# Kernel tuning notes

Measured on AMD Instinct MI355X. Metric: run time of the kernel, lower is better.

## Reference

```python
import jax, jax.numpy as jnp
import numpy as np
from jax import lax

V, E, H1, H2, D = 10000, 128, 128, 64, 64
T, B, MAXLEN = 512, 256, 30
SOS, EOS = 1, 2


def setup_inputs() -> dict:
    key = jax.random.key(0)
    ks = jax.random.split(key, 16)
    s = 0.05
    return {
        "enc_key": jax.random.normal(ks[0], (T, B, D), jnp.float32),
        "enc_values": jax.random.normal(ks[1], (T, B, D), jnp.float32),
        "mask": jax.random.randint(ks[2], (B, 1, T), 0, 2, jnp.int32),
        "emb": jax.random.normal(ks[3], (V, E), jnp.float32) * s,
        "w_ih1": jax.random.normal(ks[4], (4 * H1, E + D), jnp.float32) * s,
        "w_hh1": jax.random.normal(ks[5], (4 * H1, H1), jnp.float32) * s,
        "b_ih1": jax.random.normal(ks[6], (4 * H1,), jnp.float32) * s,
        "b_hh1": jax.random.normal(ks[7], (4 * H1,), jnp.float32) * s,
        "w_ih2": jax.random.normal(ks[8], (4 * H2, H1), jnp.float32) * s,
        "w_hh2": jax.random.normal(ks[9], (4 * H2, H2), jnp.float32) * s,
        "b_ih2": jax.random.normal(ks[10], (4 * H2,), jnp.float32) * s,
        "b_hh2": jax.random.normal(ks[11], (4 * H2,), jnp.float32) * s,
        "wq": jax.random.normal(ks[12], (D, H2), jnp.float32) * s,
        "bq": jax.random.normal(ks[13], (D,), jnp.float32) * s,
        "wp": jax.random.normal(ks[14], (V, H2 + D), jnp.float32) * s,
        "bp": jax.random.normal(ks[15], (V,), jnp.float32) * s,
    }


def _lstm_cell(x, h, c, w_ih, w_hh, b_ih, b_hh):
    # torch LSTMCell: gates ordered (i, f, g, o)
    gates = x @ w_ih.T + h @ w_hh.T + b_ih + b_hh
    i, f, g, o = jnp.split(gates, 4, axis=-1)
    c_new = jax.nn.sigmoid(f) * c + jax.nn.sigmoid(i) * jnp.tanh(g)
    h_new = jax.nn.sigmoid(o) * jnp.tanh(c_new)
    return h_new, c_new


def reference(enc_key, enc_values, mask, emb, w_ih1, w_hh1, b_ih1, b_hh1,
              w_ih2, w_hh2, b_ih2, b_hh2, wq, bq, wp, bp):
    maskf = mask.astype(enc_key.dtype)[:, 0, :]          # (B, T)
    emb_p = emb.at[EOS].set(0.0)                          # padding_idx row zeroed

    pred0 = jnp.zeros((B, V), enc_key.dtype).at[:, SOS].set(1.0)
    init = (jnp.zeros((B, H1), enc_key.dtype), jnp.zeros((B, H1), enc_key.dtype),
            jnp.zeros((B, H2), enc_key.dtype), jnp.zeros((B, H2), enc_key.dtype),
            jnp.zeros((B, D), enc_key.dtype), pred0)

    def step(carry, _):
        h1, c1, h2, c2, context, pred = carry
        tok = jnp.argmax(pred, axis=-1)                   # greedy feedback
        char_embed = emb_p[tok]                           # (B, E)
        inp = jnp.concatenate([char_embed, context], axis=1)
        h1, c1 = _lstm_cell(inp, h1, c1, w_ih1, w_hh1, b_ih1, b_hh1)
        h2, c2 = _lstm_cell(h1, h2, c2, w_ih2, w_hh2, b_ih2, b_hh2)
        query = h2 @ wq.T + bq                            # (B, D)
        energy = jnp.einsum('bd,tbd->bt', query, enc_key)
        att = jax.nn.softmax(energy, axis=-1)
        m_att = maskf * att
        m_att = m_att / jnp.clip(jnp.sum(m_att, axis=-1, keepdims=True), 2e-30, None)
        context = jnp.einsum('bt,tbd->bd', m_att, enc_values)
        pred = jnp.concatenate([h2, context], axis=1) @ wp.T + bp
        return (h1, c1, h2, c2, context, pred), pred

    _, preds = lax.scan(step, init, None, length=MAXLEN)  # (MAXLEN, B, V)
    return jnp.transpose(preds, (1, 0, 2))                # (B, MAXLEN, V)
```

## Files before the change

### kernel.cpp

```cpp
#include <hip/hip_runtime.h>
#include <hip/hip_bf16.h>

#define V 10000
#define E 128
#define H1 128
#define H2 64
#define D 64
#define T 512
#define B 256
#define MAXLEN 30
#define SOS 1
#define EOS 2
#define BGS 8
#define NVB 40

#define O_EMB   0
#define O_WIH1  1280000
#define O_WHH1  1378304
#define O_BIH1  1443840
#define O_BHH1  1444352
#define O_WIH2  1444864
#define O_WHH2  1477632
#define O_BIH2  1494016
#define O_BHH2  1494272
#define O_WQ    1494528
#define O_BQ    1498624
#define O_WP    1498688
#define O_BP    2778688
#define TOTALW  2788688

typedef unsigned long long u64;

__device__ __forceinline__ float bl(unsigned u){ return __uint_as_float(u << 16); }
__device__ __forceinline__ float bh(unsigned u){ return __uint_as_float(u & 0xFFFF0000u); }
__device__ __forceinline__ float b2f(__hip_bfloat16 x){ return __bfloat162float(x); }
__device__ __forceinline__ float sigf(float x){ return 1.f/(1.f + expf(-x)); }

__device__ __forceinline__ uint4 ldu4(const void* p){
  uint4 r; __builtin_memcpy(&r, p, 16); return r;
}
__device__ __forceinline__ float4 ldf4(const float* p){
  float4 r; __builtin_memcpy(&r, (const void*)p, 16); return r;
}
__device__ __forceinline__ float dot8b(const float* x, uint4 w){
  return x[0]*bl(w.x) + x[1]*bh(w.x) + x[2]*bl(w.y) + x[3]*bh(w.y)
       + x[4]*bl(w.z) + x[5]*bh(w.z) + x[6]*bl(w.w) + x[7]*bh(w.w);
}
__device__ __forceinline__ float dot4f(const float* x, float4 w){
  return x[0]*w.x + x[1]*w.y + x[2]*w.z + x[3]*w.w;
}

__global__ void kdtype(const void* __restrict__ probe, int* __restrict__ flagp){
  const int tid = threadIdx.x;
  const unsigned w = ((const unsigned*)probe)[tid];
  const unsigned e = (w >> 7) & 0xFFu;
  const bool inband = (e >= 0x60u) && (e <= 0x7Eu);
  const u64 m = __ballot(inband);
  if (tid == 0) flagp[0] = (m == 0xFFFFFFFFFFFFFFFFull) ? 1 : 0;
}

__global__ __launch_bounds__(256) void kcvt(
    const void* s_emb, const void* s_wih1, const void* s_whh1,
    const void* s_bih1, const void* s_bhh1, const void* s_wih2,
    const void* s_whh2, const void* s_bih2, const void* s_bhh2,
    const void* s_wq, const void* s_bq, const void* s_wp, const void* s_bp,
    float* __restrict__ dst, const int* __restrict__ flagp)
{
  const int idx = blockIdx.x * 256 + threadIdx.x;
  if (idx >= TOTALW) return;
  const int flag = flagp[0];
  const void* src; int off;
  if      (idx < O_WIH1){ src = s_emb;  off = idx - O_EMB;  }
  else if (idx < O_WHH1){ src = s_wih1; off = idx - O_WIH1; }
  else if (idx < O_BIH1){ src = s_whh1; off = idx - O_WHH1; }
  else if (idx < O_BHH1){ src = s_bih1; off = idx - O_BIH1; }
  else if (idx < O_WIH2){ src = s_bhh1; off = idx - O_BHH1; }
  else if (idx < O_WHH2){ src = s_wih2; off = idx - O_WIH2; }
  else if (idx < O_BIH2){ src = s_whh2; off = idx - O_WHH2; }
  else if (idx < O_BHH2){ src = s_bih2; off = idx - O_BIH2; }
  else if (idx < O_WQ)  { src = s_bhh2; off = idx - O_BHH2; }
  else if (idx < O_BQ)  { src = s_wq;   off = idx - O_WQ;   }
  else if (idx < O_WP)  { src = s_bq;   off = idx - O_BQ;   }
  else if (idx < O_BP)  { src = s_wp;   off = idx - O_WP;   }
  else                  { src = s_bp;   off = idx - O_BP;   }
  dst[idx] = flag ? b2f(((const __hip_bfloat16*)src)[off])
                  : ((const float*)src)[off];
}

__global__ __launch_bounds__(256) void kdec(
    int t,
    const void* __restrict__ enc_key,
    const void* __restrict__ enc_val,
    const int* __restrict__ mask,
    const float* __restrict__ emb_f,
    const float* __restrict__ wih1_f, const float* __restrict__ whh1_f,
    const float* __restrict__ bih1_f, const float* __restrict__ bhh1_f,
    const float* __restrict__ wih2_f, const float* __restrict__ whh2_f,
    const float* __restrict__ bih2_f, const float* __restrict__ bhh2_f,
    const float* __restrict__ wq_f,   const float* __restrict__ bq_f,
    float* __restrict__ h1, float* __restrict__ c1,
    float* __restrict__ h2, float* __restrict__ c2,
    float* __restrict__ ctx, float* __restrict__ xvec,
    const float* __restrict__ candv, const int* __restrict__ candi,
    const int* __restrict__ flagp)
{
  const int b = blockIdx.x;
  const int tid = threadIdx.x;
  const int flagb = flagp[0];

  __shared__ float inp_s[E + D];
  __shared__ float h1_s[H1];
  __shared__ float h2_s[H2];
  __shared__ float g_s[4*H1];
  __shared__ float q_s[D];
  __shared__ float wv_s[T];
  __shared__ float red_s[256];
  __shared__ float cv_s[NVB];
  __shared__ int   ci_s[NVB];
  __shared__ int   tok_s;

  if (t > 0 && tid < NVB){
    cv_s[tid] = candv[b*NVB + tid];
    ci_s[tid] = candi[b*NVB + tid];
  }
  __syncthreads();
  if (tid == 0){
    int tok = SOS;
    if (t > 0){
      float bv = cv_s[0]; int bi = ci_s[0];
      for (int j = 1; j < NVB; ++j)
        if (cv_s[j] > bv){ bv = cv_s[j]; bi = ci_s[j]; }
      tok = bi;
    }
    tok_s = tok;
  }
  __syncthreads();
  const int tok = tok_s;

  if (tid < E){
    inp_s[tid] = (tok == EOS) ? 0.f : emb_f[(size_t)tok*E + tid];
  } else if (tid < E + D){
    inp_s[tid] = (t == 0) ? 0.f : ctx[b*D + (tid - E)];
  }
  if (tid < H1)                h1_s[tid]       = (t == 0) ? 0.f : h1[b*H1 + tid];
  if (tid >= 128 && tid < 192) h2_s[tid - 128] = (t == 0) ? 0.f : h2[b*H2 + (tid - 128)];
  __syncthreads();

  for (int j = tid; j < 4*H1; j += 256){
    const float* wr = wih1_f + (size_t)j*(E + D);
    float acc = bih1_f[j] + bhh1_f[j];
    #pragma unroll
    for (int kk = 0; kk < (E + D)/4; ++kk) acc += dot4f(inp_s + kk*4, ldf4(wr + kk*4));
    const float* wr2 = whh1_f + (size_t)j*H1;
    #pragma unroll
    for (int kk = 0; kk < H1/4; ++kk) acc += dot4f(h1_s + kk*4, ldf4(wr2 + kk*4));
    g_s[j] = acc;
  }
  __syncthreads();

  if (tid < H1){
    float gi = sigf(g_s[tid]);
    float gf = sigf(g_s[H1 + tid]);
    float gg = tanhf(g_s[2*H1 + tid]);
    float go = sigf(g_s[3*H1 + tid]);
    float cold = (t == 0) ? 0.f : c1[b*H1 + tid];
    float cn = gf*cold + gi*gg;
    float hn = go*tanhf(cn);
    c1[b*H1 + tid] = cn;
    h1[b*H1 + tid] = hn;
    h1_s[tid] = hn;
  }
  __syncthreads();

  {
    const int j = tid;
    const float* wr = wih2_f + (size_t)j*H1;
    float acc = bih2_f[j] + bhh2_f[j];
    #pragma unroll
    for (int kk = 0; kk < H1/4; ++kk) acc += dot4f(h1_s + kk*4, ldf4(wr + kk*4));
    const float* wr2 = whh2_f + (size_t)j*H2;
    #pragma unroll
    for (int kk = 0; kk < H2/4; ++kk) acc += dot4f(h2_s + kk*4, ldf4(wr2 + kk*4));
    g_s[j] = acc;
  }
  __syncthreads();

  if (tid < H2){
    float gi = sigf(g_s[tid]);
    float gf = sigf(g_s[H2 + tid]);
    float gg = tanhf(g_s[2*H2 + tid]);
    float go = sigf(g_s[3*H2 + tid]);
    float cold = (t == 0) ? 0.f : c2[b*H2 + tid];
    float cn = gf*cold + gi*gg;
    float hn = go*tanhf(cn);
    c2[b*H2 + tid] = cn;
    h2[b*H2 + tid] = hn;
    h2_s[tid] = hn;
    xvec[b*(H2 + D) + tid] = hn;
  }
  __syncthreads();

  if (tid < D){
    const float* wr = wq_f + (size_t)tid*H2;
    float acc = bq_f[tid];
    #pragma unroll
    for (int kk = 0; kk < H2/4; ++kk) acc += dot4f(h2_s + kk*4, ldf4(wr + kk*4));
    q_s[tid] = acc;
  }
  __syncthreads();

  float e0 = 0.f, e1 = 0.f;
  if (flagb){
    const __hip_bfloat16* base = (const __hip_bfloat16*)enc_key;
    const __hip_bfloat16* kr0 = base + ((size_t)tid*B + b)*D;
    const __hip_bfloat16* kr1 = base + ((size_t)(tid + 256)*B + b)*D;
    #pragma unroll
    for (int kk = 0; kk < D/8; ++kk){
      e0 += dot8b(q_s + kk*8, ldu4(kr0 + kk*8));
      e1 += dot8b(q_s + kk*8, ldu4(kr1 + kk*8));
    }
  } else {
    const float* base = (const float*)enc_key;
    const float* kr0 = base + ((size_t)tid*B + b)*D;
    const float* kr1 = base + ((size_t)(tid + 256)*B + b)*D;
    #pragma unroll
    for (int kk = 0; kk < D/4; ++kk){
      e0 += dot4f(q_s + kk*4, ldf4(kr0 + kk*4));
      e1 += dot4f(q_s + kk*4, ldf4(kr1 + kk*4));
    }
  }
  red_s[tid] = fmaxf(e0, e1);
  __syncthreads();
  for (int s = 128; s > 0; s >>= 1){
    if (tid < s) red_s[tid] = fmaxf(red_s[tid], red_s[tid + s]);
    __syncthreads();
  }
  const float emax = red_s[0];
  __syncthreads();

  const int m0 = mask[b*T + tid], m1 = mask[b*T + tid + 256];
  const float w0 = m0 ? expf(e0 - emax) : 0.f;
  const float w1 = m1 ? expf(e1 - emax) : 0.f;
  wv_s[tid] = w0;
  wv_s[tid + 256] = w1;
  red_s[tid] = w0 + w1;
  __syncthreads();
  for (int s = 128; s > 0; s >>= 1){
    if (tid < s) red_s[tid] += red_s[tid + s];
    __syncthreads();
  }
  const float inv = 1.f / fmaxf(red_s[0], 2e-30f);
  __syncthreads();

  {
    const int d = tid & 63, ch = tid >> 6;
    float acc = 0.f;
    if (flagb){
      const __hip_bfloat16* base = (const __hip_bfloat16*)enc_val;
      for (int tt = ch*128; tt < ch*128 + 128; ++tt)
        acc += wv_s[tt] * b2f(base[((size_t)tt*B + b)*D + d]);
    } else {
      const float* base = (const float*)enc_val;
      for (int tt = ch*128; tt < ch*128 + 128; ++tt)
        acc += wv_s[tt] * base[((size_t)tt*B + b)*D + d];
    }
    red_s[tid] = acc;
  }
  __syncthreads();
  if (tid < D){
    float cv = (red_s[tid] + red_s[tid + 64] + red_s[tid + 128] + red_s[tid + 192]) * inv;
    ctx[b*D + tid] = cv;
    xvec[b*(H2 + D) + H2 + tid] = cv;
  }
}

__global__ __launch_bounds__(256) void kpred(
    int t,
    const float* __restrict__ wp_f,
    const float* __restrict__ bp_f,
    const float* __restrict__ xvec,
    void* __restrict__ outv,
    float* __restrict__ candv, int* __restrict__ candi,
    const int* __restrict__ flagp)
{
  const int tid = threadIdx.x;
  const int vb = blockIdx.x;
  const int v = vb * 256 + tid;
  const int bg = blockIdx.y;
  const int flagb = flagp[0];
  const bool valid = v < V;
  const int vc = valid ? v : 0;
  const float* wrow = wp_f + (size_t)vc*(H2 + D);
  const float* xp = xvec + (size_t)bg*BGS*(H2 + D);

  float acc[BGS];
  #pragma unroll
  for (int i = 0; i < BGS; ++i) acc[i] = 0.f;

  #pragma unroll
  for (int kk = 0; kk < (H2 + D)/4; ++kk){
    const float4 w = ldf4(wrow + kk*4);
    #pragma unroll
    for (int i = 0; i < BGS; ++i){
      const float* x = xp + i*(H2 + D) + kk*4;
      acc[i] += x[0]*w.x + x[1]*w.y + x[2]*w.z + x[3]*w.w;
    }
  }

  const float bias = valid ? bp_f[vc] : 0.f;
  #pragma unroll
  for (int i = 0; i < BGS; ++i){
    acc[i] += bias;
    if (valid){
      const size_t oi = ((size_t)(bg*BGS + i)*MAXLEN + t)*V + v;
      if (flagb) ((__hip_bfloat16*)outv)[oi] = __float2bfloat16(acc[i]);
      else       ((float*)outv)[oi] = acc[i];
    }
  }

  __shared__ float lv[4][BGS];
  __shared__ int   li[4][BGS];
  const int lane = tid & 63, wid = tid >> 6;
  #pragma unroll
  for (int i = 0; i < BGS; ++i){
    float mv = valid ? acc[i] : -__builtin_inff();
    int   mi = valid ? v : 0x7FFFFFFF;
    for (int off = 32; off > 0; off >>= 1){
      float ov = __shfl_down(mv, off);
      int   oi = __shfl_down(mi, off);
      if (ov > mv || (ov == mv && oi < mi)){ mv = ov; mi = oi; }
    }
    if (lane == 0){ lv[wid][i] = mv; li[wid][i] = mi; }
  }
  __syncthreads();
  if (tid < BGS){
    float mv = lv[0][tid]; int mi = li[0][tid];
    #pragma unroll
    for (int w2 = 1; w2 < 4; ++w2){
      float ov = lv[w2][tid]; int oi = li[w2][tid];
      if (ov > mv || (ov == mv && oi < mi)){ mv = ov; mi = oi; }
    }
    const int b = bg*BGS + tid;
    candv[b*NVB + vb] = mv;
    candi[b*NVB + vb] = mi;
  }
}

extern "C" void kernel_launch(void* const* d_in, const int* in_sizes, int n_in,
                              void* d_out, int out_size, void* d_ws, size_t ws_size,
                              hipStream_t stream)
{
  const void* enc_key = d_in[0];
  const void* enc_val = d_in[1];
  const int*  mask    = (const int*)d_in[2];
  const void* emb     = d_in[3];
  const void* w_ih1   = d_in[4];
  const void* w_hh1   = d_in[5];
  const void* b_ih1   = d_in[6];
  const void* b_hh1   = d_in[7];
  const void* w_ih2   = d_in[8];
  const void* w_hh2   = d_in[9];
  const void* b_ih2   = d_in[10];
  const void* b_hh2   = d_in[11];
  const void* wq      = d_in[12];
  const void* bq      = d_in[13];
  const void* wp      = d_in[14];
  const void* bp      = d_in[15];

  float* wsf  = (float*)d_ws;
  int*  flagp = (int*)wsf;
  float* wts  = wsf + 16;
  float* h1    = wts + TOTALW;
  float* c1    = h1   + B*H1;
  float* h2    = c1   + B*H1;
  float* c2    = h2   + B*H2;
  float* ctx   = c2   + B*H2;
  float* xvec  = ctx  + B*D;
  float* candv = xvec + B*(H2 + D);
  int*   candi = (int*)(candv + B*NVB);

  kdtype<<<dim3(1), dim3(64), 0, stream>>>(b_ih1, flagp);
  kcvt<<<dim3((TOTALW + 255)/256), dim3(256), 0, stream>>>(
      emb, w_ih1, w_hh1, b_ih1, b_hh1, w_ih2, w_hh2, b_ih2, b_hh2,
      wq, bq, wp, bp, wts, flagp);

  for (int t = 0; t < MAXLEN; ++t){
    kdec<<<dim3(B), dim3(256), 0, stream>>>(
        t, enc_key, enc_val, mask,
        wts + O_EMB,
        wts + O_WIH1, wts + O_WHH1, wts + O_BIH1, wts + O_BHH1,
        wts + O_WIH2, wts + O_WHH2, wts + O_BIH2, wts + O_BHH2,
        wts + O_WQ, wts + O_BQ,
        h1, c1, h2, c2, ctx, xvec, candv, candi, flagp);
    kpred<<<dim3(NVB, B/BGS), dim3(256), 0, stream>>>(
        t, wts + O_WP, wts + O_BP, xvec, d_out, candv, candi, flagp);
  }
}
```

Measured before the change: 3.816 ms.

## Fuse decoder steps into one persistent kernel with grid barriers

Replaces the 60 per-step launches with a single persistent kernel of 256 blocks that loops over all 30 timesteps and uses a software grid barrier between phases. The LSTM weights are partitioned across blocks and held in shared memory, so each block computes a slice of gates for a group of batch rows instead of rereading every weight row per batch. A separate pre-pass transposes the encoder keys and values to a batch-major fp32 layout for contiguous attention reads, and logits are written with nontemporal stores. The persistent design assumes all 256 blocks are co-resident and relies on a spin-wait barrier with a timeout fallback, which adds a deadlock and correctness risk.

Result: slower. 8.181 ms (+114.4%).

```diff
diff --git a/kernel.cpp b/kernel.cpp
--- a/kernel.cpp
+++ b/kernel.cpp
@@ -13,6 +13,7 @@
 #define EOS 2
 #define BGS 8
 #define NVB 40
+#define NBLK 256
 
 #define O_EMB   0
 #define O_WIH1  1280000
@@ -31,23 +32,33 @@
 
 typedef unsigned long long u64;
 
-__device__ __forceinline__ float bl(unsigned u){ return __uint_as_float(u << 16); }
-__device__ __forceinline__ float bh(unsigned u){ return __uint_as_float(u & 0xFFFF0000u); }
 __device__ __forceinline__ float b2f(__hip_bfloat16 x){ return __bfloat162float(x); }
 __device__ __forceinline__ float sigf(float x){ return 1.f/(1.f + expf(-x)); }
-
-__device__ __forceinline__ uint4 ldu4(const void* p){
-  uint4 r; __builtin_memcpy(&r, p, 16); return r;
-}
 __device__ __forceinline__ float4 ldf4(const float* p){
   float4 r; __builtin_memcpy(&r, (const void*)p, 16); return r;
 }
-__device__ __forceinline__ float dot8b(const float* x, uint4 w){
-  return x[0]*bl(w.x) + x[1]*bh(w.x) + x[2]*bl(w.y) + x[3]*bh(w.y)
-       + x[4]*bl(w.z) + x[5]*bh(w.z) + x[6]*bl(w.w) + x[7]*bh(w.w);
-}
 __device__ __forceinline__ float dot4f(const float* x, float4 w){
   return x[0]*w.x + x[1]*w.y + x[2]*w.z + x[3]*w.w;
+}
+
+__device__ __forceinline__ void gsync(unsigned* bar){
+  __syncthreads();
+  __threadfence();
+  if (threadIdx.x == 0){
+    const unsigned ticket = __hip_atomic_fetch_add(bar, 1u, __ATOMIC_ACQ_REL, __HIP_MEMORY_SCOPE_AGENT);
+    const unsigned target = ticket - (ticket % (unsigned)NBLK) + (unsigned)NBLK;
+    unsigned spins = 0u;
+    while (__hip_atomic_load(bar, __ATOMIC_RELAXED, __HIP_MEMORY_SCOPE_AGENT) < target){
+      if (__hip_atomic_load(bar + 1, __ATOMIC_RELAXED, __HIP_MEMORY_SCOPE_AGENT) != 0u) break;
+      if (++spins > 30000000u){
+        __hip_atomic_store(bar + 1, 1u, __ATOMIC_RELAXED, __HIP_MEMORY_SCOPE_AGENT);
+        break;
+      }
+      __builtin_amdgcn_s_sleep(1);
+    }
+  }
+  __syncthreads();
+  __threadfence();
 }
 
 __global__ void kdtype(const void* __restrict__ probe, int* __restrict__ flagp){
@@ -87,262 +98,333 @@
                   : ((const float*)src)[off];
 }
 
-__global__ __launch_bounds__(256) void kdec(
-    int t,
-    const void* __restrict__ enc_key,
-    const void* __restrict__ enc_val,
-    const int* __restrict__ mask,
-    const float* __restrict__ emb_f,
-    const float* __restrict__ wih1_f, const float* __restrict__ whh1_f,
-    const float* __restrict__ bih1_f, const float* __restrict__ bhh1_f,
-    const float* __restrict__ wih2_f, const float* __restrict__ whh2_f,
-    const float* __restrict__ bih2_f, const float* __restrict__ bhh2_f,
-    const float* __restrict__ wq_f,   const float* __restrict__ bq_f,
-    float* __restrict__ h1, float* __restrict__ c1,
-    float* __restrict__ h2, float* __restrict__ c2,
-    float* __restrict__ ctx, float* __restrict__ xvec,
-    const float* __restrict__ candv, const int* __restrict__ candi,
-    const int* __restrict__ flagp)
+__global__ __launch_bounds__(256) void ktrans(
+    const void* __restrict__ enc_key, const void* __restrict__ enc_val,
+    float* __restrict__ encTk, float* __restrict__ encTv,
+    const int* __restrict__ flagp, unsigned* __restrict__ bar)
 {
   const int b = blockIdx.x;
   const int tid = threadIdx.x;
+  if (b == 0 && tid < 16) bar[tid] = 0u;
+  const int flag = flagp[0];
+  const int d = tid & 63, tq = tid >> 6;
+  if (flag){
+    const __hip_bfloat16* bk = (const __hip_bfloat16*)enc_key;
+    const __hip_bfloat16* bv = (const __hip_bfloat16*)enc_val;
+    for (int tt = tq; tt < T; tt += 4){
+      encTk[((size_t)b*T + tt)*D + d] = b2f(bk[((size_t)tt*B + b)*D + d]);
+      encTv[((size_t)b*T + tt)*D + d] = b2f(bv[((size_t)tt*B + b)*D + d]);
+    }
+  } else {
+    const float* fk = (const float*)enc_key;
+    const float* fv = (const float*)enc_val;
+    for (int tt = tq; tt < T; tt += 4){
+      encTk[((size_t)b*T + tt)*D + d] = fk[((size_t)tt*B + b)*D + d];
+      encTv[((size_t)b*T + tt)*D + d] = fv[((size_t)tt*B + b)*D + d];
+    }
+  }
+}
+
+__global__ __launch_bounds__(256) void kmain(
+    const float* __restrict__ wts,
+    const float* __restrict__ encTk, const float* __restrict__ encTv,
+    const int* __restrict__ mask,
+    void* __restrict__ outv,
+    float* __restrict__ h1g,
+    float* __restrict__ h2g,
+    float* __restrict__ ctxg,
+    float* __restrict__ candv, int* __restrict__ candi,
+    unsigned* __restrict__ bar, const int* __restrict__ flagp)
+{
+  const int bid = blockIdx.x;
+  const int tid = threadIdx.x;
   const int flagb = flagp[0];
 
-  __shared__ float inp_s[E + D];
-  __shared__ float h1_s[H1];
-  __shared__ float h2_s[H2];
-  __shared__ float g_s[4*H1];
+  const int rt  = bid >> 5;
+  const int bA  = (bid & 31) * 8;
+  const int rt2 = bid >> 6;
+  const int bB  = (bid & 63) * 4;
+
+  __shared__ float4 wA4[80*64];
+  __shared__ float4 wB4[48*64];
+  __shared__ __align__(16) float xs[8*324];
+  __shared__ __align__(16) float x2s[4*196];
+  __shared__ float g_s[64*8];
+  __shared__ float c1_s[16*8];
+  __shared__ float c2_s[16*4];
+  __shared__ float bias1_s[64], bias2_s[64];
   __shared__ float q_s[D];
+  __shared__ float h2b_s[H2];
   __shared__ float wv_s[T];
   __shared__ float red_s[256];
-  __shared__ float cv_s[NVB];
-  __shared__ int   ci_s[NVB];
-  __shared__ int   tok_s;
-
-  if (t > 0 && tid < NVB){
-    cv_s[tid] = candv[b*NVB + tid];
-    ci_s[tid] = candi[b*NVB + tid];
-  }
-  __syncthreads();
-  if (tid == 0){
-    int tok = SOS;
+  __shared__ float lv_s[4*8]; __shared__ int li_s[4*8];
+  __shared__ int tok_s[8];
+
+  for (int idx = tid; idx < 80*64; idx += 256){
+    const int k4 = idx >> 6, r = idx & 63;
+    const int row = ((r >> 4) * 128) + (rt * 16) + (r & 15);
+    float4 w;
+    if (k4 < 48) w = ldf4(wts + O_WIH1 + (size_t)row*(E+D) + k4*4);
+    else         w = ldf4(wts + O_WHH1 + (size_t)row*H1 + (k4-48)*4);
+    wA4[idx] = w;
+  }
+  for (int idx = tid; idx < 48*64; idx += 256){
+    const int k4 = idx >> 6, r = idx & 63;
+    const int row = ((r >> 4) * 64) + (rt2 * 16) + (r & 15);
+    float4 w;
+    if (k4 < 32) w = ldf4(wts + O_WIH2 + (size_t)row*H1 + k4*4);
+    else         w = ldf4(wts + O_WHH2 + (size_t)row*H2 + (k4-32)*4);
+    wB4[idx] = w;
+  }
+  if (tid < 64){
+    const int rowA = ((tid >> 4) * 128) + (rt * 16) + (tid & 15);
+    bias1_s[tid] = wts[O_BIH1 + rowA] + wts[O_BHH1 + rowA];
+    const int rowB = ((tid >> 4) * 64) + (rt2 * 16) + (tid & 15);
+    bias2_s[tid] = wts[O_BIH2 + rowB] + wts[O_BHH2 + rowB];
+  }
+  if (tid < 128) c1_s[tid] = 0.f;
+  if (tid < 64)  c2_s[tid] = 0.f;
+  {
+    const int b = bid;
+    if (tid < H1) h1g[(size_t)B*H1 + (size_t)b*H1 + tid] = 0.f;
+    if (tid < H2) h2g[(size_t)B*H2 + (size_t)b*H2 + tid] = 0.f;
+    if (tid < D)  ctxg[(size_t)b*D + tid] = 0.f;
+  }
+  gsync(bar);
+
+  for (int t = 0; t < MAXLEN; ++t){
+    const int par = t & 1;
+    const float* h1prev = h1g + (size_t)(par^1)*B*H1;
+    float*       h1new  = h1g + (size_t)par*B*H1;
+    const float* h2prev = h2g + (size_t)(par^1)*B*H2;
+    float*       h2new  = h2g + (size_t)par*B*H2;
+
     if (t > 0){
-      float bv = cv_s[0]; int bi = ci_s[0];
-      for (int j = 1; j < NVB; ++j)
-        if (cv_s[j] > bv){ bv = cv_s[j]; bi = ci_s[j]; }
-      tok = bi;
-    }
-    tok_s = tok;
-  }
-  __syncthreads();
-  const int tok = tok_s;
-
-  if (tid < E){
-    inp_s[tid] = (tok == EOS) ? 0.f : emb_f[(size_t)tok*E + tid];
-  } else if (tid < E + D){
-    inp_s[tid] = (t == 0) ? 0.f : ctx[b*D + (tid - E)];
-  }
-  if (tid < H1)                h1_s[tid]       = (t == 0) ? 0.f : h1[b*H1 + tid];
-  if (tid >= 128 && tid < 192) h2_s[tid - 128] = (t == 0) ? 0.f : h2[b*H2 + (tid - 128)];
-  __syncthreads();
-
-  for (int j = tid; j < 4*H1; j += 256){
-    const float* wr = wih1_f + (size_t)j*(E + D);
-    float acc = bih1_f[j] + bhh1_f[j];
-    #pragma unroll
-    for (int kk = 0; kk < (E + D)/4; ++kk) acc += dot4f(inp_s + kk*4, ldf4(wr + kk*4));
-    const float* wr2 = whh1_f + (size_t)j*H1;
-    #pragma unroll
-    for (int kk = 0; kk < H1/4; ++kk) acc += dot4f(h1_s + kk*4, ldf4(wr2 + kk*4));
-    g_s[j] = acc;
-  }
-  __syncthreads();
-
-  if (tid < H1){
-    float gi = sigf(g_s[tid]);
-    float gf = sigf(g_s[H1 + tid]);
-    float gg = tanhf(g_s[2*H1 + tid]);
-    float go = sigf(g_s[3*H1 + tid]);
-    float cold = (t == 0) ? 0.f : c1[b*H1 + tid];
-    float cn = gf*cold + gi*gg;
-    float hn = go*tanhf(cn);
-    c1[b*H1 + tid] = cn;
-    h1[b*H1 + tid] = hn;
-    h1_s[tid] = hn;
-  }
-  __syncthreads();
-
-  {
-    const int j = tid;
-    const float* wr = wih2_f + (size_t)j*H1;
-    float acc = bih2_f[j] + bhh2_f[j];
-    #pragma unroll
-    for (int kk = 0; kk < H1/4; ++kk) acc += dot4f(h1_s + kk*4, ldf4(wr + kk*4));
-    const float* wr2 = whh2_f + (size_t)j*H2;
-    #pragma unroll
-    for (int kk = 0; kk < H2/4; ++kk) acc += dot4f(h2_s + kk*4, ldf4(wr2 + kk*4));
-    g_s[j] = acc;
-  }
-  __syncthreads();
-
-  if (tid < H2){
-    float gi = sigf(g_s[tid]);
-    float gf = sigf(g_s[H2 + tid]);
-    float gg = tanhf(g_s[2*H2 + tid]);
-    float go = sigf(g_s[3*H2 + tid]);
-    float cold = (t == 0) ? 0.f : c2[b*H2 + tid];
-    float cn = gf*cold + gi*gg;
-    float hn = go*tanhf(cn);
-    c2[b*H2 + tid] = cn;
-    h2[b*H2 + tid] = hn;
-    h2_s[tid] = hn;
-    xvec[b*(H2 + D) + tid] = hn;
-  }
-  __syncthreads();
-
-  if (tid < D){
-    const float* wr = wq_f + (size_t)tid*H2;
-    float acc = bq_f[tid];
-    #pragma unroll
-    for (int kk = 0; kk < H2/4; ++kk) acc += dot4f(h2_s + kk*4, ldf4(wr + kk*4));
-    q_s[tid] = acc;
-  }
-  __syncthreads();
-
-  float e0 = 0.f, e1 = 0.f;
-  if (flagb){
-    const __hip_bfloat16* base = (const __hip_bfloat16*)enc_key;
-    const __hip_bfloat16* kr0 = base + ((size_t)tid*B + b)*D;
-    const __hip_bfloat16* kr1 = base + ((size_t)(tid + 256)*B + b)*D;
-    #pragma unroll
-    for (int kk = 0; kk < D/8; ++kk){
-      e0 += dot8b(q_s + kk*8, ldu4(kr0 + kk*8));
-      e1 += dot8b(q_s + kk*8, ldu4(kr1 + kk*8));
-    }
-  } else {
-    const float* base = (const float*)enc_key;
-    const float* kr0 = base + ((size_t)tid*B + b)*D;
-    const float* kr1 = base + ((size_t)(tid + 256)*B + b)*D;
-    #pragma unroll
-    for (int kk = 0; kk < D/4; ++kk){
-      e0 += dot4f(q_s + kk*4, ldf4(kr0 + kk*4));
-      e1 += dot4f(q_s + kk*4, ldf4(kr1 + kk*4));
-    }
-  }
-  red_s[tid] = fmaxf(e0, e1);
-  __syncthreads();
-  for (int s = 128; s > 0; s >>= 1){
-    if (tid < s) red_s[tid] = fmaxf(red_s[tid], red_s[tid + s]);
+      const int bi = tid >> 5, j = tid & 31;
+      const int b = bA + bi;
+      float mv = candv[b*NVB + j];
+      int   mi = candi[b*NVB + j];
+      if (j < NVB - 32){
+        float ov = candv[b*NVB + j + 32]; int oi = candi[b*NVB + j + 32];
+        if (ov > mv || (ov == mv && oi < mi)){ mv = ov; mi = oi; }
+      }
+      #pragma unroll
+      for (int off = 16; off > 0; off >>= 1){
+        float ov = __shfl_down(mv, off); int oi = __shfl_down(mi, off);
+        if (ov > mv || (ov == mv && oi < mi)){ mv = ov; mi = oi; }
+      }
+      if (j == 0) tok_s[bi] = mi;
+    } else {
+      if (tid < 8) tok_s[tid] = SOS;
+    }
     __syncthreads();
-  }
-  const float emax = red_s[0];
-  __syncthreads();
-
-  const int m0 = mask[b*T + tid], m1 = mask[b*T + tid + 256];
-  const float w0 = m0 ? expf(e0 - emax) : 0.f;
-  const float w1 = m1 ? expf(e1 - emax) : 0.f;
-  wv_s[tid] = w0;
-  wv_s[tid + 256] = w1;
-  red_s[tid] = w0 + w1;
-  __syncthreads();
-  for (int s = 128; s > 0; s >>= 1){
-    if (tid < s) red_s[tid] += red_s[tid + s];
+
+    for (int bi = 0; bi < 8; ++bi){
+      const int b = bA + bi;
+      const int tok = tok_s[bi];
+      for (int k = tid; k < 320; k += 256){
+        float x;
+        if (k < E)          x = (tok == EOS) ? 0.f : wts[O_EMB + (size_t)tok*E + k];
+        else if (k < E + D) x = ctxg[(size_t)b*D + (k - E)];
+        else                x = h1prev[(size_t)b*H1 + (k - (E + D))];
+        xs[bi*324 + k] = x;
+      }
+    }
     __syncthreads();
-  }
-  const float inv = 1.f / fmaxf(red_s[0], 2e-30f);
-  __syncthreads();
-
-  {
-    const int d = tid & 63, ch = tid >> 6;
-    float acc = 0.f;
-    if (flagb){
-      const __hip_bfloat16* base = (const __hip_bfloat16*)enc_val;
-      for (int tt = ch*128; tt < ch*128 + 128; ++tt)
-        acc += wv_s[tt] * b2f(base[((size_t)tt*B + b)*D + d]);
-    } else {
-      const float* base = (const float*)enc_val;
-      for (int tt = ch*128; tt < ch*128 + 128; ++tt)
-        acc += wv_s[tt] * base[((size_t)tt*B + b)*D + d];
-    }
-    red_s[tid] = acc;
-  }
-  __syncthreads();
-  if (tid < D){
-    float cv = (red_s[tid] + red_s[tid + 64] + red_s[tid + 128] + red_s[tid + 192]) * inv;
-    ctx[b*D + tid] = cv;
-    xvec[b*(H2 + D) + H2 + tid] = cv;
-  }
-}
-
-__global__ __launch_bounds__(256) void kpred(
-    int t,
-    const float* __restrict__ wp_f,
-    const float* __restrict__ bp_f,
-    const float* __restrict__ xvec,
-    void* __restrict__ outv,
-    float* __restrict__ candv, int* __restrict__ candi,
-    const int* __restrict__ flagp)
-{
-  const int tid = threadIdx.x;
-  const int vb = blockIdx.x;
-  const int v = vb * 256 + tid;
-  const int bg = blockIdx.y;
-  const int flagb = flagp[0];
-  const bool valid = v < V;
-  const int vc = valid ? v : 0;
-  const float* wrow = wp_f + (size_t)vc*(H2 + D);
-  const float* xp = xvec + (size_t)bg*BGS*(H2 + D);
-
-  float acc[BGS];
-  #pragma unroll
-  for (int i = 0; i < BGS; ++i) acc[i] = 0.f;
-
-  #pragma unroll
-  for (int kk = 0; kk < (H2 + D)/4; ++kk){
-    const float4 w = ldf4(wrow + kk*4);
-    #pragma unroll
-    for (int i = 0; i < BGS; ++i){
-      const float* x = xp + i*(H2 + D) + kk*4;
-      acc[i] += x[0]*w.x + x[1]*w.y + x[2]*w.z + x[3]*w.w;
-    }
-  }
-
-  const float bias = valid ? bp_f[vc] : 0.f;
-  #pragma unroll
-  for (int i = 0; i < BGS; ++i){
-    acc[i] += bias;
-    if (valid){
-      const size_t oi = ((size_t)(bg*BGS + i)*MAXLEN + t)*V + v;
-      if (flagb) ((__hip_bfloat16*)outv)[oi] = __float2bfloat16(acc[i]);
-      else       ((float*)outv)[oi] = acc[i];
-    }
-  }
-
-  __shared__ float lv[4][BGS];
-  __shared__ int   li[4][BGS];
-  const int lane = tid & 63, wid = tid >> 6;
-  #pragma unroll
-  for (int i = 0; i < BGS; ++i){
-    float mv = valid ? acc[i] : -__builtin_inff();
-    int   mi = valid ? v : 0x7FFFFFFF;
-    for (int off = 32; off > 0; off >>= 1){
-      float ov = __shfl_down(mv, off);
-      int   oi = __shfl_down(mi, off);
-      if (ov > mv || (ov == mv && oi < mi)){ mv = ov; mi = oi; }
-    }
-    if (lane == 0){ lv[wid][i] = mv; li[wid][i] = mi; }
-  }
-  __syncthreads();
-  if (tid < BGS){
-    float mv = lv[0][tid]; int mi = li[0][tid];
-    #pragma unroll
-    for (int w2 = 1; w2 < 4; ++w2){
-      float ov = lv[w2][tid]; int oi = li[w2][tid];
-      if (ov > mv || (ov == mv && oi < mi)){ mv = ov; mi = oi; }
-    }
-    const int b = bg*BGS + tid;
-    candv[b*NVB + vb] = mv;
-    candi[b*NVB + vb] = mi;
+
+    {
+      const int r = tid >> 2, bq = tid & 3;
+      const float4* x0 = (const float4*)(xs + (bq*2    )*324);
+      const float4* x1 = (const float4*)(xs + (bq*2 + 1)*324);
+      float a0 = bias1_s[r], a1 = a0;
+      #pragma unroll 8
+      for (int k4 = 0; k4 < 80; ++k4){
+        const float4 w = wA4[k4*64 + r];
+        const float4 xa = x0[k4], xb = x1[k4];
+        a0 += xa.x*w.x + xa.y*w.y + xa.z*w.z + xa.w*w.w;
+        a1 += xb.x*w.x + xb.y*w.y + xb.z*w.z + xb.w*w.w;
+      }
+      g_s[r*8 + bq*2]     = a0;
+      g_s[r*8 + bq*2 + 1] = a1;
+    }
+    __syncthreads();
+    if (tid < 128){
+      const int ui = tid >> 3, bi = tid & 7;
+      const float gi = sigf (g_s[(ui     )*8 + bi]);
+      const float gf = sigf (g_s[(16 + ui)*8 + bi]);
+      const float gg = tanhf(g_s[(32 + ui)*8 + bi]);
+      const float go = sigf (g_s[(48 + ui)*8 + bi]);
+      const float cn = gf * c1_s[ui*8 + bi] + gi * gg;
+      c1_s[ui*8 + bi] = cn;
+      h1new[(size_t)(bA + bi)*H1 + rt*16 + ui] = go * tanhf(cn);
+    }
+    gsync(bar);
+
+    {
+      const int bi = tid >> 6, k0 = tid & 63;
+      #pragma unroll
+      for (int kk = k0; kk < 192; kk += 64){
+        float x = (kk < H1) ? h1new[(size_t)(bB + bi)*H1 + kk]
+                            : h2prev[(size_t)(bB + bi)*H2 + (kk - H1)];
+        x2s[bi*196 + kk] = x;
+      }
+    }
+    __syncthreads();
+    {
+      const int r = tid >> 2, bq = tid & 3;
+      const float4* xp = (const float4*)(x2s + bq*196);
+      float a = bias2_s[r];
+      #pragma unroll 8
+      for (int k4 = 0; k4 < 48; ++k4){
+        const float4 w = wB4[k4*64 + r];
+        const float4 x = xp[k4];
+        a += x.x*w.x + x.y*w.y + x.z*w.z + x.w*w.w;
+      }
+      g_s[r*8 + bq] = a;
+    }
+    __syncthreads();
+    if (tid < 64){
+      const int ui = tid >> 2, bi = tid & 3;
+      const float gi = sigf (g_s[(ui     )*8 + bi]);
+      const float gf = sigf (g_s[(16 + ui)*8 + bi]);
+      const float gg = tanhf(g_s[(32 + ui)*8 + bi]);
+      const float go = sigf (g_s[(48 + ui)*8 + bi]);
+      const float cn = gf * c2_s[ui*4 + bi] + gi * gg;
+      c2_s[ui*4 + bi] = cn;
+      h2new[(size_t)(bB + bi)*H2 + rt2*16 + ui] = go * tanhf(cn);
+    }
+    gsync(bar);
+
+    {
+      const int b = bid;
+      if (tid < H2) h2b_s[tid] = h2new[(size_t)b*H2 + tid];
+      __syncthreads();
+      if (tid < D){
+        const float* wr = wts + O_WQ + (size_t)tid*H2;
+        float acc = wts[O_BQ + tid];
+        #pragma unroll
+        for (int kk = 0; kk < H2/4; ++kk) acc += dot4f(h2b_s + kk*4, ldf4(wr + kk*4));
+        q_s[tid] = acc;
+      }
+      __syncthreads();
+      float e0 = 0.f, e1 = 0.f;
+      const float* kr0 = encTk + ((size_t)b*T + tid)*D;
+      const float* kr1 = kr0 + (size_t)256*D;
+      #pragma unroll
+      for (int kk = 0; kk < D/4; ++kk){
+        e0 += dot4f(q_s + kk*4, ldf4(kr0 + kk*4));
+        e1 += dot4f(q_s + kk*4, ldf4(kr1 + kk*4));
+      }
+      red_s[tid] = fmaxf(e0, e1);
+      __syncthreads();
+      for (int s = 128; s > 0; s >>= 1){
+        if (tid < s) red_s[tid] = fmaxf(red_s[tid], red_s[tid + s]);
+        __syncthreads();
+      }
+      const float emax = red_s[0];
+      __syncthreads();
+      const int m0 = mask[b*T + tid], m1 = mask[b*T + tid + 256];
+      const float w0 = m0 ? expf(e0 - emax) : 0.f;
+      const float w1 = m1 ? expf(e1 - emax) : 0.f;
+      wv_s[tid] = w0;
+      wv_s[tid + 256] = w1;
+      red_s[tid] = w0 + w1;
+      __syncthreads();
+      for (int s = 128; s > 0; s >>= 1){
+        if (tid < s) red_s[tid] += red_s[tid + s];
+        __syncthreads();
+      }
+      const float inv = 1.f / fmaxf(red_s[0], 2e-30f);
+      __syncthreads();
+      {
+        const int d = tid & 63, ch = tid >> 6;
+        const float* vb2 = encTv + (size_t)b*T*D + d;
+        float acc = 0.f;
+        #pragma unroll 8
+        for (int tt = ch*128; tt < ch*128 + 128; ++tt)
+          acc += wv_s[tt] * vb2[(size_t)tt*D];
+        red_s[tid] = acc;
+      }
+      __syncthreads();
+      if (tid < D)
+        ctxg[(size_t)b*D + tid] =
+            (red_s[tid] + red_s[tid+64] + red_s[tid+128] + red_s[tid+192]) * inv;
+    }
+    gsync(bar);
+
+    for (int i = 0; i < 5; ++i){
+      const int tau = i*256 + bid;
+      const int vb = tau % NVB;
+      const int bg = tau / NVB;
+      {
+        const int bi = tid >> 5, kq = tid & 31;
+        const int b = bg*BGS + bi;
+        const int k = kq * 4;
+        float4 x;
+        if (k < H2) x = ldf4(h2new + (size_t)b*H2 + k);
+        else        x = ldf4(ctxg + (size_t)b*D + (k - H2));
+        *(float4*)(xs + bi*324 + k) = x;
+      }
+      __syncthreads();
+
+      const int v = vb*256 + tid;
+      const bool valid = v < V;
+      const int vc = valid ? v : 0;
+      const float* wrow = wts + O_WP + (size_t)vc*(H2 + D);
+      float acc[BGS];
+      #pragma unroll
+      for (int q = 0; q < BGS; ++q) acc[q] = 0.f;
+      #pragma unroll 8
+      for (int kk = 0; kk < (H2 + D)/4; ++kk){
+        const float4 w = ldf4(wrow + kk*4);
+        #pragma unroll
+        for (int q = 0; q < BGS; ++q){
+          const float4 x = *(const float4*)(xs + q*324 + kk*4);
+          acc[q] += x.x*w.x + x.y*w.y + x.z*w.z + x.w*w.w;
+        }
+      }
+      const float bias = valid ? wts[O_BP + vc] : 0.f;
+      #pragma unroll
+      for (int q = 0; q < BGS; ++q){
+        acc[q] += bias;
+        if (valid){
+          const size_t oi = ((size_t)(bg*BGS + q)*MAXLEN + t)*V + v;
+          if (flagb){
+            __hip_bfloat16 hv = __float2bfloat16(acc[q]);
+            unsigned short us; __builtin_memcpy(&us, &hv, 2);
+            __builtin_nontemporal_store(us, (unsigned short*)outv + oi);
+          } else {
+            __builtin_nontemporal_store(acc[q], (float*)outv + oi);
+          }
+        }
+      }
+      const int lane = tid & 63, wid = tid >> 6;
+      #pragma unroll
+      for (int q = 0; q < BGS; ++q){
+        float mv = valid ? acc[q] : -__builtin_inff();
+        int   mi = valid ? v : 0x7FFFFFFF;
+        for (int off = 32; off > 0; off >>= 1){
+          float ov = __shfl_down(mv, off);
+          int   oi = __shfl_down(mi, off);
+          if (ov > mv || (ov == mv && oi < mi)){ mv = ov; mi = oi; }
+        }
+        if (lane == 0){ lv_s[wid*8 + q] = mv; li_s[wid*8 + q] = mi; }
+      }
+      __syncthreads();
+      if (tid < BGS){
+        float mv = lv_s[tid]; int mi = li_s[tid];
+        #pragma unroll
+        for (int w2 = 1; w2 < 4; ++w2){
+          float ov = lv_s[w2*8 + tid]; int oi = li_s[w2*8 + tid];
+          if (ov > mv || (ov == mv && oi < mi)){ mv = ov; mi = oi; }
+        }
+        const int b = bg*BGS + tid;
+        candv[b*NVB + vb] = mv;
+        candi[b*NVB + vb] = mi;
+      }
+      __syncthreads();
+    }
+    gsync(bar);
   }
 }
 
@@ -370,29 +452,22 @@
   float* wsf  = (float*)d_ws;
   int*  flagp = (int*)wsf;
   float* wts  = wsf + 16;
-  float* h1    = wts + TOTALW;
-  float* c1    = h1   + B*H1;
-  float* h2    = c1   + B*H1;
-  float* c2    = h2   + B*H2;
-  float* ctx   = c2   + B*H2;
-  float* xvec  = ctx  + B*D;
-  float* candv = xvec + B*(H2 + D);
+  float* h1g   = wts + TOTALW;
+  float* h2g   = h1g + 2*B*H1;
+  float* ctxg  = h2g + 2*B*H2;
+  float* candv = ctxg + B*D;
   int*   candi = (int*)(candv + B*NVB);
+  unsigned* bar = (unsigned*)(candi + B*NVB);
+  float* encTk = (float*)(bar + 16);
+  float* encTv = encTk + (size_t)B*T*D;
 
   kdtype<<<dim3(1), dim3(64), 0, stream>>>(b_ih1, flagp);
   kcvt<<<dim3((TOTALW + 255)/256), dim3(256), 0, stream>>>(
       emb, w_ih1, w_hh1, b_ih1, b_hh1, w_ih2, w_hh2, b_ih2, b_hh2,
       wq, bq, wp, bp, wts, flagp);
-
-  for (int t = 0; t < MAXLEN; ++t){
-    kdec<<<dim3(B), dim3(256), 0, stream>>>(
-        t, enc_key, enc_val, mask,
-        wts + O_EMB,
-        wts + O_WIH1, wts + O_WHH1, wts + O_BIH1, wts + O_BHH1,
-        wts + O_WIH2, wts + O_WHH2, wts + O_BIH2, wts + O_BHH2,
-        wts + O_WQ, wts + O_BQ,
-        h1, c1, h2, c2, ctx, xvec, candv, candi, flagp);
-    kpred<<<dim3(NVB, B/BGS), dim3(256), 0, stream>>>(
-        t, wts + O_WP, wts + O_BP, xvec, d_out, candv, candi, flagp);
-  }
-}
+  ktrans<<<dim3(B), dim3(256), 0, stream>>>(enc_key, enc_val, encTk, encTv, flagp, bar);
+
+  kmain<<<dim3(NBLK), dim3(256), 0, stream>>>(
+      wts, encTk, encTv, mask, d_out,
+      h1g, h2g, ctxg, candv, candi, bar, flagp);
+}
```
